# Performance work log

Measured on AMD Instinct MI355X. Metric: run time of the kernel, lower is better.

Reference implementation:

```python
import jax, jax.numpy as jnp
import numpy as np

S, B, C, H = 8192, 4, 512, 8
D = C // H
EPS = 1e-6


def setup_inputs() -> dict:
    key = jax.random.key(0)
    ks = jax.random.split(key, 11)
    scale = 1.0 / np.sqrt(C)
    return {
        "query": jax.random.normal(ks[0], (S, B, C), jnp.float32),
        "key": jax.random.normal(ks[1], (S, B, C), jnp.float32),
        "value": jax.random.normal(ks[2], (S, B, C), jnp.float32),
        "Wq": jax.random.normal(ks[3], (C, C), jnp.float32) * scale,
        "bq": jnp.zeros((C,), jnp.float32),
        "Wk": jax.random.normal(ks[4], (C, C), jnp.float32) * scale,
        "bk": jnp.zeros((C,), jnp.float32),
        "Wv": jax.random.normal(ks[5], (C, C), jnp.float32) * scale,
        "bv": jnp.zeros((C,), jnp.float32),
        "Wp": jax.random.normal(ks[6], (C, C), jnp.float32) * scale,
        "bp": jnp.zeros((C,), jnp.float32),
    }


def _elu_fm(x):
    # ELU(x) + 1 feature map
    return jax.nn.elu(x) + 1.0


def _heads(x, W, b):
    # x: [B, N, C] -> [B, H, N, D]
    y = x @ W.T + b
    Bb, N, _ = y.shape
    return y.reshape(Bb, N, H, D).transpose(0, 2, 1, 3)


def reference(query, key, value, Wq, bq, Wk, bk, Wv, bv, Wp, bp):
    # inputs [S, B, C] -> batch-first [B, S, C]
    q_in = query.transpose(1, 0, 2)
    k_in = key.transpose(1, 0, 2)
    v_in = value.transpose(1, 0, 2)

    q = _elu_fm(_heads(q_in, Wq, bq))   # [B,H,N,D]
    k = _elu_fm(_heads(k_in, Wk, bk))   # [B,H,N,D]
    v = _heads(v_in, Wv, bv)            # [B,H,N,D]

    # linear attention: O(N) kv-sum formulation
    kv = jnp.einsum('bhnd,bhnf->bhdf', k, v)       # [B,H,D,D]
    k_sum = k.sum(axis=2)                          # [B,H,D]
    qkv = jnp.einsum('bhnd,bhdf->bhnf', q, kv)     # [B,H,N,D]
    denom = jnp.einsum('bhnd,bhd->bhn', q, k_sum)  # [B,H,N]
    y = qkv / (denom[..., None] + EPS)

    # merge heads, output projection, back to [S, B, C]
    y = y.transpose(0, 2, 1, 3).reshape(q_in.shape[0], q_in.shape[1], C)
    out = y @ Wp.T + bp
    return out.transpose(1, 0, 2)
```

## Files before the change

kernel.cpp:

```cpp
#include <hip/hip_runtime.h>
#include <hip/hip_bf16.h>
#include <math.h>

#define S_LEN 8192
#define BATCH 4
#define CDIM  512
#define HEADS 8
#define DDIM  64
#define MROWS (S_LEN * BATCH)
#define EPS_F 1e-6f

typedef __attribute__((ext_vector_type(8))) short     short8_t;
typedef __attribute__((ext_vector_type(4))) float     f32x4;
typedef unsigned short ushort_t;
typedef __attribute__((ext_vector_type(8))) unsigned short ushort8_t;

static __device__ __forceinline__ ushort_t f2bf(float f) {
  __hip_bfloat16 h = __float2bfloat16(f);
  return *(ushort_t*)&h;
}

static __device__ __forceinline__ void gl2lds16(const ushort_t* g, ushort_t* l) {
  __builtin_amdgcn_global_load_lds((const __attribute__((address_space(1))) void*)g,
                                   (__attribute__((address_space(3))) void*)l,
                                   16, 0, 0);
}

#define WAIT_VM12 asm volatile("s_waitcnt vmcnt(12) lgkmcnt(0)" ::: "memory")
#define WAIT_VM8  asm volatile("s_waitcnt vmcnt(8) lgkmcnt(0)"  ::: "memory")
#define WAIT_VM4  asm volatile("s_waitcnt vmcnt(4) lgkmcnt(0)"  ::: "memory")
#define WAIT_VM0  asm volatile("s_waitcnt vmcnt(0) lgkmcnt(0)"  ::: "memory")

__global__ __launch_bounds__(256)
void cvtW_pack(const float* __restrict__ a, const float* __restrict__ b,
               const float* __restrict__ c, const float* __restrict__ d,
               ushort_t* __restrict__ oa, ushort_t* __restrict__ ob,
               ushort_t* __restrict__ oc, ushort_t* __restrict__ od) {
  const float* src = (blockIdx.y == 0) ? a : (blockIdx.y == 1) ? b :
                     (blockIdx.y == 2) ? c : d;
  ushort_t* dst    = (blockIdx.y == 0) ? oa : (blockIdx.y == 1) ? ob :
                     (blockIdx.y == 2) ? oc : od;
  const size_t i = ((size_t)blockIdx.x * 256 + threadIdx.x) * 8;
  const int n  = (int)(i >> 9);
  const int k0 = (int)(i & 511);
  const float4 x = *(const float4*)&src[i];
  const float4 y = *(const float4*)&src[i + 4];
  ushort8_t p;
  p[0] = f2bf(x.x); p[1] = f2bf(x.y); p[2] = f2bf(x.z); p[3] = f2bf(x.w);
  p[4] = f2bf(y.x); p[5] = f2bf(y.y); p[6] = f2bf(y.z); p[7] = f2bf(y.w);
  const int kf   = k0 >> 5;
  const int lane = ((k0 >> 3) & 3) * 16 + (n & 15);
  const int nfg  = n >> 4;
  *(ushort8_t*)&dst[(((size_t)nfg * 16 + kf) * 64 + lane) * 8] = p;
}

template<int AF32, int OUTF32>
static __device__ __forceinline__
void gemm256_body(const void* __restrict__ Av, const ushort_t* __restrict__ Wpk,
                  const float* __restrict__ bias, void* __restrict__ Yv,
                  const bool act, const int m0, const int n0, ushort_t* lds) {
  const int t    = threadIdx.x;
  const int w    = t >> 6;
  const int lane = t & 63;
  const int lr   = lane & 15;
  const int lk8  = (lane >> 4) * 8;
  const int wm   = (w >> 2) * 128;
  const int wn   = (w & 3) * 64;

  const float*    Xf = (const float*)Av;
  const ushort_t* Ah = (const ushort_t*)Av;

  ushort_t* A0 = lds;
  ushort_t* A1 = lds + 16384;
  ushort_t* B0 = lds + 32768;
  ushort_t* B1 = lds + 49152;

  f32x4 ar[4][2];

  auto regloadA = [&](int kt) {
    #pragma unroll
    for (int j = 0; j < 4; ++j) {
      const int fid = w * 4 + j;
      const size_t g = (size_t)(m0 + (fid >> 1) * 16 + lr) * CDIM +
                       kt + (fid & 1) * 32 + lk8;
      ar[j][0] = __builtin_nontemporal_load((const f32x4*)&Xf[g]);
      ar[j][1] = __builtin_nontemporal_load((const f32x4*)&Xf[g + 4]);
    }
  };
  auto stageA_f32 = [&](ushort_t* Ab) {
    #pragma unroll
    for (int j = 0; j < 4; ++j) {
      const int fid = w * 4 + j;
      short8_t v;
      v[0] = (short)f2bf(ar[j][0][0]); v[1] = (short)f2bf(ar[j][0][1]);
      v[2] = (short)f2bf(ar[j][0][2]); v[3] = (short)f2bf(ar[j][0][3]);
      v[4] = (short)f2bf(ar[j][1][0]); v[5] = (short)f2bf(ar[j][1][1]);
      v[6] = (short)f2bf(ar[j][1][2]); v[7] = (short)f2bf(ar[j][1][3]);
      *(short8_t*)&Ab[(size_t)fid * 512 + lane * 8] = v;
    }
  };
  auto stageA_bf16 = [&](ushort_t* Ab, int kt) {
    #pragma unroll
    for (int j = 0; j < 4; ++j) {
      const int fid = w * 4 + j;
      const ushort_t* g = Ah + (size_t)(m0 + (fid >> 1) * 16 + lr) * CDIM +
                          kt + (fid & 1) * 32 + lk8;
      gl2lds16(g, &Ab[fid * 512]);
    }
  };
  auto stageB = [&](ushort_t* Bb, int kt) {
    #pragma unroll
    for (int j = 0; j < 4; ++j) {
      const int fid = w * 4 + j;
      const size_t idx = ((size_t)((n0 >> 4) + (fid >> 1)) * 16 +
                          (kt >> 5) + (fid & 1));
      gl2lds16(Wpk + idx * 512 + lane * 8, &Bb[fid * 512]);
    }
  };

  f32x4 acc[8][4];
  #pragma unroll
  for (int mf = 0; mf < 8; ++mf)
    #pragma unroll
    for (int nf = 0; nf < 4; ++nf)
      acc[mf][nf] = (f32x4){0.f, 0.f, 0.f, 0.f};

  auto compute = [&](const ushort_t* Ab, const ushort_t* Bb) {
    short8_t bfr[2][4];
    #pragma unroll
    for (int kf = 0; kf < 2; ++kf)
      #pragma unroll
      for (int nf = 0; nf < 4; ++nf) {
        const int fidb = ((wn >> 4) + nf) * 2 + kf;
        bfr[kf][nf] = *(const short8_t*)&Bb[fidb * 512 + lane * 8];
      }
    __builtin_amdgcn_s_setprio(1);
    #pragma unroll
    for (int mf = 0; mf < 8; ++mf) {
      const int fa = ((wm >> 4) + mf) * 2;
      const short8_t a0 = *(const short8_t*)&Ab[(fa + 0) * 512 + lane * 8];
      const short8_t a1 = *(const short8_t*)&Ab[(fa + 1) * 512 + lane * 8];
      #pragma unroll
      for (int nf = 0; nf < 4; ++nf)
        acc[mf][nf] = __builtin_amdgcn_mfma_f32_16x16x32_bf16(
            a0, bfr[0][nf], acc[mf][nf], 0, 0, 0);
      #pragma unroll
      for (int nf = 0; nf < 4; ++nf)
        acc[mf][nf] = __builtin_amdgcn_mfma_f32_16x16x32_bf16(
            a1, bfr[1][nf], acc[mf][nf], 0, 0, 0);
    }
    __builtin_amdgcn_s_setprio(0);
  };

  if (AF32) {
    regloadA(0);
    stageA_f32(A0);
    stageB(B0, 0);
    regloadA(64);
  } else {
    stageA_bf16(A0, 0);
    stageB(B0, 0);
  }

#define KSTEP(ks, WAITM)                                                   \
  do {                                                                     \
    ushort_t* curA = ((ks) & 1) ? A1 : A0;                                 \
    ushort_t* curB = ((ks) & 1) ? B1 : B0;                                 \
    ushort_t* nxtA = ((ks) & 1) ? A0 : A1;                                 \
    ushort_t* nxtB = ((ks) & 1) ? B0 : B1;                                 \
    if ((ks) < 7) {                                                        \
      if (AF32) {                                                          \
        stageA_f32(nxtA);                                                  \
        if ((ks) + 2 < 8) regloadA(((ks) + 2) * 64);                       \
      } else {                                                             \
        stageA_bf16(nxtA, ((ks) + 1) * 64);                                \
      }                                                                    \
      stageB(nxtB, ((ks) + 1) * 64);                                       \
    }                                                                      \
    WAITM;                                                                 \
    __builtin_amdgcn_s_barrier();                                          \
    __builtin_amdgcn_sched_barrier(0);                                     \
    compute(curA, curB);                                                   \
    __builtin_amdgcn_s_barrier();                                          \
  } while (0)

  if (AF32) {
    KSTEP(0, WAIT_VM12); KSTEP(1, WAIT_VM12); KSTEP(2, WAIT_VM12);
    KSTEP(3, WAIT_VM12); KSTEP(4, WAIT_VM12); KSTEP(5, WAIT_VM12);
    KSTEP(6, WAIT_VM4);  KSTEP(7, WAIT_VM0);
  } else {
    KSTEP(0, WAIT_VM8); KSTEP(1, WAIT_VM8); KSTEP(2, WAIT_VM8);
    KSTEP(3, WAIT_VM8); KSTEP(4, WAIT_VM8); KSTEP(5, WAIT_VM8);
    KSTEP(6, WAIT_VM8); KSTEP(7, WAIT_VM0);
  }
#undef KSTEP

  if (OUTF32) {
    float* Yf = (float*)Yv;
    #pragma unroll
    for (int nf = 0; nf < 4; ++nf) {
      const int col = n0 + wn + nf * 16 + lr;
      const float bi = bias[col];
      #pragma unroll
      for (int mf = 0; mf < 8; ++mf) {
        #pragma unroll
        for (int r = 0; r < 4; ++r) {
          const int m = m0 + wm + mf * 16 + (lane >> 4) * 4 + r;
          __builtin_nontemporal_store(acc[mf][nf][r] + bi,
                                      &Yf[(size_t)m * CDIM + col]);
        }
      }
    }
  } else {
    ushort_t* Yh = (ushort_t*)Yv;
    #pragma unroll
    for (int nf = 0; nf < 4; ++nf) {
      const int col = wn + nf * 16 + lr;
      const float bi = bias[n0 + col];
      #pragma unroll
      for (int mf = 0; mf < 8; ++mf) {
        #pragma unroll
        for (int r = 0; r < 4; ++r) {
          const int row = wm + mf * 16 + (lane >> 4) * 4 + r;
          float vv = acc[mf][nf][r] + bi;
          if (act) vv = (vv > 0.f) ? (vv + 1.f) : expf(vv);
          lds[row * 256 + col] = f2bf(vv);
        }
      }
    }
    __syncthreads();
    #pragma unroll
    for (int it = 0; it < 16; ++it) {
      const int u   = it * 512 + t;
      const int row = u >> 5;
      const int c8  = (u & 31) * 8;
      const short8_t v = *(const short8_t*)&lds[u * 8];
      __builtin_nontemporal_store(
          v, (short8_t*)&Yh[(size_t)(m0 + row) * CDIM + n0 + c8]);
    }
  }
}

__global__ __launch_bounds__(512)
void proj3_256(const float* __restrict__ Xq, const float* __restrict__ Xk,
               const float* __restrict__ Xv,
               const ushort_t* __restrict__ Wqp, const ushort_t* __restrict__ Wkp,
               const ushort_t* __restrict__ Wvp,
               const float* __restrict__ bq, const float* __restrict__ bk,
               const float* __restrict__ bv,
               ushort_t* __restrict__ Yq, ushort_t* __restrict__ Yk,
               ushort_t* __restrict__ Yv) {
  extern __shared__ ushort_t lds[];
  const int z = blockIdx.z;
  const float*    X    = (z == 0) ? Xq : (z == 1) ? Xk : Xv;
  const ushort_t* Wpk  = (z == 0) ? Wqp : (z == 1) ? Wkp : Wvp;
  const float*    bias = (z == 0) ? bq : (z == 1) ? bk : bv;
  ushort_t*       Y    = (z == 0) ? Yq : (z == 1) ? Yk : Yv;
  gemm256_body<1, 0>(X, Wpk, bias, Y, z < 2,
                     blockIdx.y * 256, blockIdx.x * 256, lds);
}

__global__ __launch_bounds__(512)
void outp_256(const ushort_t* __restrict__ A, const ushort_t* __restrict__ Wpk,
              const float* __restrict__ bias, float* __restrict__ Y) {
  extern __shared__ ushort_t lds[];
  gemm256_body<0, 1>(A, Wpk, bias, Y, false,
                     blockIdx.y * 256, blockIdx.x * 256, lds);
}

__global__ __launch_bounds__(256)
void gemm_kv(const ushort_t* __restrict__ Kb, const ushort_t* __restrict__ Vb,
             float* __restrict__ kvpart, float* __restrict__ ksumpart) {
  __shared__ __align__(16) ushort_t klds[8192];
  __shared__ __align__(16) ushort_t vlds[8192];
  const int bh    = blockIdx.x;
  const int chunk = blockIdx.y;
  const int b = bh >> 3, h = bh & 7;
  const int t = threadIdx.x;
  const int w = t >> 6;
  const int lane = t & 63;

  f32x4 acc[4];
  #pragma unroll
  for (int fg = 0; fg < 4; ++fg) acc[fg] = (f32x4){0.f, 0.f, 0.f, 0.f};
  f32x4 accs = (f32x4){0.f, 0.f, 0.f, 0.f};

  short8_t ones;
  #pragma unroll
  for (int i = 0; i < 8; ++i) ones[i] = (short)0x3F80;

  for (int round = 0; round < 4; ++round) {
    const int sbase = chunk * 512 + round * 128;
    __syncthreads();
    #pragma unroll
    for (int i = 0; i < 4; ++i) {
      const int idx  = i * 256 + t;
      const int sl   = idx >> 3;
      const int d8   = idx & 7;
      const size_t src = (size_t)((sbase + sl) * BATCH + b) * CDIM + h * DDIM + d8 * 8;
      const ushort8_t kp = *(const ushort8_t*)&Kb[src];
      const ushort8_t vp = *(const ushort8_t*)&Vb[src];
      const int sb  = sl >> 5;
      const int j   = sl & 7;
      const int lp0 = (d8 & 1) * 8 + ((sl >> 3) & 3) * 16;
      const int dg  = d8 >> 1;
      const int kbase = ((sb * 4 + dg) * 64 + lp0) * 8 + j;
      #pragma unroll
      for (int e = 0; e < 8; ++e) {
        klds[kbase + e * 8] = kp[e];
        vlds[kbase + e * 8] = vp[e];
      }
    }
    __syncthreads();
    #pragma unroll
    for (int sb = 0; sb < 4; ++sb) {
      const short8_t af = *(const short8_t*)&klds[((sb * 4 + w) * 64 + lane) * 8];
      accs = __builtin_amdgcn_mfma_f32_16x16x32_bf16(af, ones, accs, 0, 0, 0);
      #pragma unroll
      for (int fg = 0; fg < 4; ++fg) {
        const short8_t bf = *(const short8_t*)&vlds[((sb * 4 + fg) * 64 + lane) * 8];
        acc[fg] = __builtin_amdgcn_mfma_f32_16x16x32_bf16(af, bf, acc[fg], 0, 0, 0);
      }
    }
  }

  const size_t obase = ((size_t)bh * 16 + chunk) * 64;
  #pragma unroll
  for (int fg = 0; fg < 4; ++fg)
    #pragma unroll
    for (int r = 0; r < 4; ++r) {
      const int d = w * 16 + (lane >> 4) * 4 + r;
      kvpart[(obase + d) * 64 + fg * 16 + (lane & 15)] = acc[fg][r];
    }
  if ((lane & 15) == 0) {
    #pragma unroll
    for (int r = 0; r < 4; ++r)
      ksumpart[obase + w * 16 + (lane >> 4) * 4 + r] = accs[r];
  }
}

__global__ __launch_bounds__(256)
void kv_finish(const float* __restrict__ kvpart, const float* __restrict__ ksumpart,
               ushort_t* __restrict__ kvT) {
  const int bh = blockIdx.x;
  const int t  = threadIdx.x;
  for (int idx = t; idx < 4096; idx += 256) {
    const int d = idx >> 6, f = idx & 63;
    float s = 0.f;
    for (int c = 0; c < 16; ++c)
      s += kvpart[(((size_t)bh * 16 + c) * 64 + d) * 64 + f];
    kvT[((size_t)bh * 80 + f) * 64 + d] = f2bf(s);
  }
  if (t < 64) {
    float s = 0.f;
    for (int c = 0; c < 16; ++c)
      s += ksumpart[((size_t)bh * 16 + c) * 64 + t];
    kvT[((size_t)bh * 80 + 64) * 64 + t] = f2bf(s);
  }
  for (int i = t; i < 15 * 64; i += 256)
    kvT[((size_t)bh * 80 + 65) * 64 + i] = 0;
}

__global__ __launch_bounds__(256)
void gemm_qkv(ushort_t* __restrict__ Qb, const ushort_t* __restrict__ kvT) {
  __shared__ __align__(16) ushort_t alds[8192];
  __shared__ __align__(16) ushort_t blds[5120];
  const int bh    = blockIdx.x;
  const int chunk = blockIdx.y;
  const int b = bh >> 3, h = bh & 7;
  const int t = threadIdx.x;
  const int w = t >> 6;
  const int lane = t & 63;
  const int lr = lane & 15;
  const int lk = (lane >> 4) * 8;

  #pragma unroll
  for (int i = 0; i < 4; ++i) {
    const int fidx = w * 4 + i;
    const int ks = fidx >> 3, fm = fidx & 7;
    const ushort_t* src = Qb +
        (size_t)((chunk * 128 + fm * 16 + lr) * BATCH + b) * CDIM +
        h * DDIM + ks * 32 + lk;
    gl2lds16(src, &alds[fidx * 512]);
  }
  for (int idx = w; idx < 10; idx += 4) {
    const int ks = idx / 5, fg = idx % 5;
    const ushort_t* src = kvT + (size_t)(bh * 80 + fg * 16 + lr) * 64 + ks * 32 + lk;
    gl2lds16(src, &blds[idx * 512]);
  }
  __syncthreads();

  f32x4 acc[2][5];
  #pragma unroll
  for (int mi = 0; mi < 2; ++mi)
    #pragma unroll
    for (int fg = 0; fg < 5; ++fg)
      acc[mi][fg] = (f32x4){0.f, 0.f, 0.f, 0.f};

  #pragma unroll
  for (int ks = 0; ks < 2; ++ks) {
    short8_t af[2], bf[5];
    #pragma unroll
    for (int mi = 0; mi < 2; ++mi)
      af[mi] = *(const short8_t*)&alds[(ks * 8 + w * 2 + mi) * 512 + lane * 8];
    #pragma unroll
    for (int fg = 0; fg < 5; ++fg)
      bf[fg] = *(const short8_t*)&blds[(ks * 5 + fg) * 512 + lane * 8];
    #pragma unroll
    for (int mi = 0; mi < 2; ++mi)
      #pragma unroll
      for (int fg = 0; fg < 5; ++fg)
        acc[mi][fg] = __builtin_amdgcn_mfma_f32_16x16x32_bf16(
            af[mi], bf[fg], acc[mi][fg], 0, 0, 0);
  }

  #pragma unroll
  for (int mi = 0; mi < 2; ++mi) {
    #pragma unroll
    for (int r = 0; r < 4; ++r) {
      const float dv  = __shfl(acc[mi][4][r], lane & 48);
      const float inv = 1.f / (dv + EPS_F);
      const int s = chunk * 128 + w * 32 + mi * 16 + (lane >> 4) * 4 + r;
      const size_t rowb = (size_t)(s * BATCH + b) * CDIM + h * DDIM;
      #pragma unroll
      for (int fg = 0; fg < 4; ++fg)
        Qb[rowb + fg * 16 + lr] = f2bf(acc[mi][fg][r] * inv);
    }
  }
}

extern "C" void kernel_launch(void* const* d_in, const int* in_sizes, int n_in,
                              void* d_out, int out_size, void* d_ws, size_t ws_size,
                              hipStream_t stream) {
  const float* q_in = (const float*)d_in[0];
  const float* k_in = (const float*)d_in[1];
  const float* v_in = (const float*)d_in[2];
  const float* Wq   = (const float*)d_in[3];
  const float* bq   = (const float*)d_in[4];
  const float* Wk   = (const float*)d_in[5];
  const float* bk   = (const float*)d_in[6];
  const float* Wv   = (const float*)d_in[7];
  const float* bv   = (const float*)d_in[8];
  const float* Wp   = (const float*)d_in[9];
  const float* bp   = (const float*)d_in[10];
  float* out = (float*)d_out;

  const size_t NTOK = (size_t)MROWS * CDIM;
  const size_t NW   = (size_t)CDIM * CDIM;
  ushort_t* Wqp    = (ushort_t*)d_ws;
  ushort_t* Wkp    = Wqp + NW;
  ushort_t* Wvp    = Wkp + NW;
  ushort_t* Wpp    = Wvp + NW;
  ushort_t* qbuf   = Wpp + NW;
  ushort_t* kbuf   = qbuf + NTOK;
  ushort_t* vbuf   = kbuf + NTOK;
  ushort_t* kvT    = vbuf + NTOK;
  float* kvpart    = (float*)(kvT + (size_t)32 * 80 * 64);
  float* ksumpart  = kvpart + (size_t)512 * 64 * 64;

  const dim3 blk(256);
  const size_t LDSB = 131072;

  cvtW_pack<<<dim3(128, 4), blk, 0, stream>>>(Wq, Wk, Wv, Wp,
                                              Wqp, Wkp, Wvp, Wpp);

  proj3_256<<<dim3(CDIM / 256, MROWS / 256, 3), dim3(512), LDSB, stream>>>(
      q_in, k_in, v_in, Wqp, Wkp, Wvp, bq, bk, bv, qbuf, kbuf, vbuf);

  gemm_kv<<<dim3(32, 16), blk, 0, stream>>>(kbuf, vbuf, kvpart, ksumpart);
  kv_finish<<<dim3(32), blk, 0, stream>>>(kvpart, ksumpart, kvT);

  gemm_qkv<<<dim3(32, 64), blk, 0, stream>>>(qbuf, kvT);

  outp_256<<<dim3(CDIM / 256, MROWS / 256), dim3(512), LDSB, stream>>>(
      qbuf, Wpp, bp, out);
}
```

Baseline: 241.4 us.

## Shrink projection GEMM tiles to 128x128 with 256 threads and K=32 steps

```diff
diff --git a/kernel.cpp b/kernel.cpp
--- a/kernel.cpp
+++ b/kernel.cpp
@@ -26,10 +26,7 @@
                                    16, 0, 0);
 }
 
-#define WAIT_VM12 asm volatile("s_waitcnt vmcnt(12) lgkmcnt(0)" ::: "memory")
-#define WAIT_VM8  asm volatile("s_waitcnt vmcnt(8) lgkmcnt(0)"  ::: "memory")
-#define WAIT_VM4  asm volatile("s_waitcnt vmcnt(4) lgkmcnt(0)"  ::: "memory")
-#define WAIT_VM0  asm volatile("s_waitcnt vmcnt(0) lgkmcnt(0)"  ::: "memory")
+#define WAIT_VM(N) asm volatile("s_waitcnt vmcnt(" #N ") lgkmcnt(0)" ::: "memory")
 
 __global__ __launch_bounds__(256)
 void cvtW_pack(const float* __restrict__ a, const float* __restrict__ b,
@@ -56,7 +53,7 @@
 
 template<int AF32, int OUTF32>
 static __device__ __forceinline__
-void gemm256_body(const void* __restrict__ Av, const ushort_t* __restrict__ Wpk,
+void gemm128_body(const void* __restrict__ Av, const ushort_t* __restrict__ Wpk,
                   const float* __restrict__ bias, void* __restrict__ Yv,
                   const bool act, const int m0, const int n0, ushort_t* lds) {
   const int t    = threadIdx.x;
@@ -64,134 +61,129 @@
   const int lane = t & 63;
   const int lr   = lane & 15;
   const int lk8  = (lane >> 4) * 8;
-  const int wm   = (w >> 2) * 128;
-  const int wn   = (w & 3) * 64;
+  const int wm   = (w >> 1) * 64;
+  const int wn   = (w & 1) * 64;
 
   const float*    Xf = (const float*)Av;
   const ushort_t* Ah = (const ushort_t*)Av;
 
-  ushort_t* A0 = lds;
-  ushort_t* A1 = lds + 16384;
-  ushort_t* B0 = lds + 32768;
-  ushort_t* B1 = lds + 49152;
-
-  f32x4 ar[4][2];
-
-  auto regloadA = [&](int kt) {
-    #pragma unroll
-    for (int j = 0; j < 4; ++j) {
-      const int fid = w * 4 + j;
-      const size_t g = (size_t)(m0 + (fid >> 1) * 16 + lr) * CDIM +
-                       kt + (fid & 1) * 32 + lk8;
-      ar[j][0] = __builtin_nontemporal_load((const f32x4*)&Xf[g]);
-      ar[j][1] = __builtin_nontemporal_load((const f32x4*)&Xf[g + 4]);
+  ushort_t* Ab[2] = { lds,        lds + 4096 };
+  ushort_t* Bb[2] = { lds + 8192, lds + 12288 };
+
+  f32x4 ar[2][2][2];
+
+  auto regloadA = [&](int set, int kt) {
+    #pragma unroll
+    for (int j = 0; j < 2; ++j) {
+      const int fid = w * 2 + j;
+      const size_t g = (size_t)(m0 + fid * 16 + lr) * CDIM + kt + lk8;
+      if (set == 0) {
+        ar[0][j][0] = __builtin_nontemporal_load((const f32x4*)&Xf[g]);
+        ar[0][j][1] = __builtin_nontemporal_load((const f32x4*)&Xf[g + 4]);
+      } else {
+        ar[1][j][0] = __builtin_nontemporal_load((const f32x4*)&Xf[g]);
+        ar[1][j][1] = __builtin_nontemporal_load((const f32x4*)&Xf[g + 4]);
+      }
     }
   };
-  auto stageA_f32 = [&](ushort_t* Ab) {
-    #pragma unroll
-    for (int j = 0; j < 4; ++j) {
-      const int fid = w * 4 + j;
+  auto stageA_f32 = [&](int set, ushort_t* A_) {
+    #pragma unroll
+    for (int j = 0; j < 2; ++j) {
+      const int fid = w * 2 + j;
+      const f32x4 x0 = set ? ar[1][j][0] : ar[0][j][0];
+      const f32x4 x1 = set ? ar[1][j][1] : ar[0][j][1];
       short8_t v;
-      v[0] = (short)f2bf(ar[j][0][0]); v[1] = (short)f2bf(ar[j][0][1]);
-      v[2] = (short)f2bf(ar[j][0][2]); v[3] = (short)f2bf(ar[j][0][3]);
-      v[4] = (short)f2bf(ar[j][1][0]); v[5] = (short)f2bf(ar[j][1][1]);
-      v[6] = (short)f2bf(ar[j][1][2]); v[7] = (short)f2bf(ar[j][1][3]);
-      *(short8_t*)&Ab[(size_t)fid * 512 + lane * 8] = v;
+      v[0] = (short)f2bf(x0[0]); v[1] = (short)f2bf(x0[1]);
+      v[2] = (short)f2bf(x0[2]); v[3] = (short)f2bf(x0[3]);
+      v[4] = (short)f2bf(x1[0]); v[5] = (short)f2bf(x1[1]);
+      v[6] = (short)f2bf(x1[2]); v[7] = (short)f2bf(x1[3]);
+      *(short8_t*)&A_[(size_t)fid * 512 + lane * 8] = v;
     }
   };
-  auto stageA_bf16 = [&](ushort_t* Ab, int kt) {
-    #pragma unroll
-    for (int j = 0; j < 4; ++j) {
-      const int fid = w * 4 + j;
-      const ushort_t* g = Ah + (size_t)(m0 + (fid >> 1) * 16 + lr) * CDIM +
-                          kt + (fid & 1) * 32 + lk8;
-      gl2lds16(g, &Ab[fid * 512]);
+  auto stageA_bf16 = [&](ushort_t* A_, int kt) {
+    #pragma unroll
+    for (int j = 0; j < 2; ++j) {
+      const int fid = w * 2 + j;
+      const ushort_t* g = Ah + (size_t)(m0 + fid * 16 + lr) * CDIM + kt + lk8;
+      gl2lds16(g, &A_[fid * 512]);
     }
   };
-  auto stageB = [&](ushort_t* Bb, int kt) {
-    #pragma unroll
-    for (int j = 0; j < 4; ++j) {
-      const int fid = w * 4 + j;
-      const size_t idx = ((size_t)((n0 >> 4) + (fid >> 1)) * 16 +
-                          (kt >> 5) + (fid & 1));
-      gl2lds16(Wpk + idx * 512 + lane * 8, &Bb[fid * 512]);
+  auto stageB = [&](ushort_t* B_, int kt) {
+    #pragma unroll
+    for (int j = 0; j < 2; ++j) {
+      const int fid = w * 2 + j;
+      const size_t idx = (size_t)((n0 >> 4) + fid) * 16 + (kt >> 5);
+      gl2lds16(Wpk + idx * 512 + lane * 8, &B_[fid * 512]);
     }
   };
 
-  f32x4 acc[8][4];
-  #pragma unroll
-  for (int mf = 0; mf < 8; ++mf)
+  f32x4 acc[4][4];
+  #pragma unroll
+  for (int mf = 0; mf < 4; ++mf)
     #pragma unroll
     for (int nf = 0; nf < 4; ++nf)
       acc[mf][nf] = (f32x4){0.f, 0.f, 0.f, 0.f};
 
-  auto compute = [&](const ushort_t* Ab, const ushort_t* Bb) {
-    short8_t bfr[2][4];
-    #pragma unroll
-    for (int kf = 0; kf < 2; ++kf)
-      #pragma unroll
-      for (int nf = 0; nf < 4; ++nf) {
-        const int fidb = ((wn >> 4) + nf) * 2 + kf;
-        bfr[kf][nf] = *(const short8_t*)&Bb[fidb * 512 + lane * 8];
-      }
+  auto compute = [&](const ushort_t* A_, const ushort_t* B_) {
+    short8_t afr[4], bfr[4];
+    #pragma unroll
+    for (int nf = 0; nf < 4; ++nf)
+      bfr[nf] = *(const short8_t*)&B_[((wn >> 4) + nf) * 512 + lane * 8];
+    #pragma unroll
+    for (int mf = 0; mf < 4; ++mf)
+      afr[mf] = *(const short8_t*)&A_[((wm >> 4) + mf) * 512 + lane * 8];
     __builtin_amdgcn_s_setprio(1);
     #pragma unroll
-    for (int mf = 0; mf < 8; ++mf) {
-      const int fa = ((wm >> 4) + mf) * 2;
-      const short8_t a0 = *(const short8_t*)&Ab[(fa + 0) * 512 + lane * 8];
-      const short8_t a1 = *(const short8_t*)&Ab[(fa + 1) * 512 + lane * 8];
+    for (int mf = 0; mf < 4; ++mf)
       #pragma unroll
       for (int nf = 0; nf < 4; ++nf)
         acc[mf][nf] = __builtin_amdgcn_mfma_f32_16x16x32_bf16(
-            a0, bfr[0][nf], acc[mf][nf], 0, 0, 0);
-      #pragma unroll
-      for (int nf = 0; nf < 4; ++nf)
-        acc[mf][nf] = __builtin_amdgcn_mfma_f32_16x16x32_bf16(
-            a1, bfr[1][nf], acc[mf][nf], 0, 0, 0);
-    }
+            afr[mf], bfr[nf], acc[mf][nf], 0, 0, 0);
     __builtin_amdgcn_s_setprio(0);
   };
 
   if (AF32) {
-    regloadA(0);
-    stageA_f32(A0);
-    stageB(B0, 0);
-    regloadA(64);
+    regloadA(0, 0);
+    stageA_f32(0, Ab[0]);
+    stageB(Bb[0], 0);
+    regloadA(1, 32);
+    regloadA(0, 64);
   } else {
-    stageA_bf16(A0, 0);
-    stageB(B0, 0);
-  }
-
-#define KSTEP(ks, WAITM)                                                   \
+    stageA_bf16(Ab[0], 0);
+    stageB(Bb[0], 0);
+  }
+  __builtin_amdgcn_sched_barrier(0);
+
+#define KSTEP(ks, WN)                                                      \
   do {                                                                     \
-    ushort_t* curA = ((ks) & 1) ? A1 : A0;                                 \
-    ushort_t* curB = ((ks) & 1) ? B1 : B0;                                 \
-    ushort_t* nxtA = ((ks) & 1) ? A0 : A1;                                 \
-    ushort_t* nxtB = ((ks) & 1) ? B0 : B1;                                 \
-    if ((ks) < 7) {                                                        \
+    if ((ks) <= 14) {                                                      \
       if (AF32) {                                                          \
-        stageA_f32(nxtA);                                                  \
-        if ((ks) + 2 < 8) regloadA(((ks) + 2) * 64);                       \
+        stageA_f32(((ks) + 1) & 1, Ab[((ks) + 1) & 1]);                    \
+        stageB(Bb[((ks) + 1) & 1], ((ks) + 1) * 32);                       \
+        if ((ks) <= 12) regloadA(((ks) + 1) & 1, ((ks) + 3) * 32);         \
       } else {                                                             \
-        stageA_bf16(nxtA, ((ks) + 1) * 64);                                \
+        stageA_bf16(Ab[((ks) + 1) & 1], ((ks) + 1) * 32);                  \
+        stageB(Bb[((ks) + 1) & 1], ((ks) + 1) * 32);                       \
       }                                                                    \
-      stageB(nxtB, ((ks) + 1) * 64);                                       \
     }                                                                      \
-    WAITM;                                                                 \
+    __builtin_amdgcn_sched_barrier(0);                                     \
+    WAIT_VM(WN);                                                           \
     __builtin_amdgcn_s_barrier();                                          \
     __builtin_amdgcn_sched_barrier(0);                                     \
-    compute(curA, curB);                                                   \
+    compute(Ab[(ks) & 1], Bb[(ks) & 1]);                                   \
     __builtin_amdgcn_s_barrier();                                          \
   } while (0)
 
   if (AF32) {
-    KSTEP(0, WAIT_VM12); KSTEP(1, WAIT_VM12); KSTEP(2, WAIT_VM12);
-    KSTEP(3, WAIT_VM12); KSTEP(4, WAIT_VM12); KSTEP(5, WAIT_VM12);
-    KSTEP(6, WAIT_VM4);  KSTEP(7, WAIT_VM0);
+    KSTEP(0, 10);  KSTEP(1, 10);  KSTEP(2, 10);  KSTEP(3, 10);
+    KSTEP(4, 10);  KSTEP(5, 10);  KSTEP(6, 10);  KSTEP(7, 10);
+    KSTEP(8, 10);  KSTEP(9, 10);  KSTEP(10, 10); KSTEP(11, 10);
+    KSTEP(12, 10); KSTEP(13, 6);  KSTEP(14, 2);  KSTEP(15, 0);
   } else {
-    KSTEP(0, WAIT_VM8); KSTEP(1, WAIT_VM8); KSTEP(2, WAIT_VM8);
-    KSTEP(3, WAIT_VM8); KSTEP(4, WAIT_VM8); KSTEP(5, WAIT_VM8);
-    KSTEP(6, WAIT_VM8); KSTEP(7, WAIT_VM0);
+    KSTEP(0, 4);  KSTEP(1, 4);  KSTEP(2, 4);  KSTEP(3, 4);
+    KSTEP(4, 4);  KSTEP(5, 4);  KSTEP(6, 4);  KSTEP(7, 4);
+    KSTEP(8, 4);  KSTEP(9, 4);  KSTEP(10, 4); KSTEP(11, 4);
+    KSTEP(12, 4); KSTEP(13, 4); KSTEP(14, 4); KSTEP(15, 0);
   }
 #undef KSTEP
 
@@ -202,7 +194,7 @@
       const int col = n0 + wn + nf * 16 + lr;
       const float bi = bias[col];
       #pragma unroll
-      for (int mf = 0; mf < 8; ++mf) {
+      for (int mf = 0; mf < 4; ++mf) {
         #pragma unroll
         for (int r = 0; r < 4; ++r) {
           const int m = m0 + wm + mf * 16 + (lane >> 4) * 4 + r;
@@ -218,22 +210,22 @@
       const int col = wn + nf * 16 + lr;
       const float bi = bias[n0 + col];
       #pragma unroll
-      for (int mf = 0; mf < 8; ++mf) {
+      for (int mf = 0; mf < 4; ++mf) {
         #pragma unroll
         for (int r = 0; r < 4; ++r) {
           const int row = wm + mf * 16 + (lane >> 4) * 4 + r;
           float vv = acc[mf][nf][r] + bi;
           if (act) vv = (vv > 0.f) ? (vv + 1.f) : expf(vv);
-          lds[row * 256 + col] = f2bf(vv);
+          lds[row * 128 + col] = f2bf(vv);
         }
       }
     }
     __syncthreads();
     #pragma unroll
-    for (int it = 0; it < 16; ++it) {
-      const int u   = it * 512 + t;
-      const int row = u >> 5;
-      const int c8  = (u & 31) * 8;
+    for (int it = 0; it < 8; ++it) {
+      const int u   = it * 256 + t;
+      const int row = u >> 4;
+      const int c8  = (u & 15) * 8;
       const short8_t v = *(const short8_t*)&lds[u * 8];
       __builtin_nontemporal_store(
           v, (short8_t*)&Yh[(size_t)(m0 + row) * CDIM + n0 + c8]);
@@ -241,8 +233,8 @@
   }
 }
 
-__global__ __launch_bounds__(512)
-void proj3_256(const float* __restrict__ Xq, const float* __restrict__ Xk,
+__global__ __launch_bounds__(256)
+void proj3_128(const float* __restrict__ Xq, const float* __restrict__ Xk,
                const float* __restrict__ Xv,
                const ushort_t* __restrict__ Wqp, const ushort_t* __restrict__ Wkp,
                const ushort_t* __restrict__ Wvp,
@@ -250,22 +242,22 @@
                const float* __restrict__ bv,
                ushort_t* __restrict__ Yq, ushort_t* __restrict__ Yk,
                ushort_t* __restrict__ Yv) {
-  extern __shared__ ushort_t lds[];
+  __shared__ __align__(16) ushort_t lds[16384];
   const int z = blockIdx.z;
   const float*    X    = (z == 0) ? Xq : (z == 1) ? Xk : Xv;
   const ushort_t* Wpk  = (z == 0) ? Wqp : (z == 1) ? Wkp : Wvp;
   const float*    bias = (z == 0) ? bq : (z == 1) ? bk : bv;
   ushort_t*       Y    = (z == 0) ? Yq : (z == 1) ? Yk : Yv;
-  gemm256_body<1, 0>(X, Wpk, bias, Y, z < 2,
-                     blockIdx.y * 256, blockIdx.x * 256, lds);
-}
-
-__global__ __launch_bounds__(512)
-void outp_256(const ushort_t* __restrict__ A, const ushort_t* __restrict__ Wpk,
+  gemm128_body<1, 0>(X, Wpk, bias, Y, z < 2,
+                     blockIdx.x * 128, blockIdx.y * 128, lds);
+}
+
+__global__ __launch_bounds__(256)
+void outp_128(const ushort_t* __restrict__ A, const ushort_t* __restrict__ Wpk,
               const float* __restrict__ bias, float* __restrict__ Y) {
-  extern __shared__ ushort_t lds[];
-  gemm256_body<0, 1>(A, Wpk, bias, Y, false,
-                     blockIdx.y * 256, blockIdx.x * 256, lds);
+  __shared__ __align__(16) ushort_t lds[16384];
+  gemm128_body<0, 1>(A, Wpk, bias, Y, false,
+                     blockIdx.x * 128, blockIdx.y * 128, lds);
 }
 
 __global__ __launch_bounds__(256)
@@ -459,12 +451,11 @@
   float* ksumpart  = kvpart + (size_t)512 * 64 * 64;
 
   const dim3 blk(256);
-  const size_t LDSB = 131072;
 
   cvtW_pack<<<dim3(128, 4), blk, 0, stream>>>(Wq, Wk, Wv, Wp,
                                               Wqp, Wkp, Wvp, Wpp);
 
-  proj3_256<<<dim3(CDIM / 256, MROWS / 256, 3), dim3(512), LDSB, stream>>>(
+  proj3_128<<<dim3(MROWS / 128, CDIM / 128, 3), blk, 0, stream>>>(
       q_in, k_in, v_in, Wqp, Wkp, Wvp, bq, bk, bv, qbuf, kbuf, vbuf);
 
   gemm_kv<<<dim3(32, 16), blk, 0, stream>>>(kbuf, vbuf, kvpart, ksumpart);
@@ -472,6 +463,6 @@
 
   gemm_qkv<<<dim3(32, 64), blk, 0, stream>>>(qbuf, kvT);
 
-  outp_256<<<dim3(CDIM / 256, MROWS / 256), dim3(512), LDSB, stream>>>(
+  outp_128<<<dim3(MROWS / 128, CDIM / 128), blk, 0, stream>>>(
       qbuf, Wpp, bp, out);
 }
```

New measurement: 283.2 us. 17.3% more time.
